# Kernel optimization log

Hardware: AMD Instinct MI355X
Metric: run time of the kernel (lower is better)

Reference implementation:

```python
import jax, jax.numpy as jnp
import numpy as np

HEADS = 4
RATES = (1, 2, 3, 4)
BN_EPS = 1e-5


def setup_inputs() -> dict:
    key = jax.random.key(0)
    k1, k2, k3 = jax.random.split(key, 3)
    b, c, h, w = 4, 256, 128, 128
    x = jax.random.normal(k1, (b, c, h, w), dtype=jnp.float32)
    w_qkv = jax.random.normal(k2, (3 * c, c), dtype=jnp.float32) * 0.02
    w_proj = jax.random.normal(k3, (c, c), dtype=jnp.float32) * 0.02
    gamma = jnp.ones((c,), dtype=jnp.float32)
    beta = jnp.zeros((c,), dtype=jnp.float32)
    return {"x": x, "w_qkv": w_qkv, "w_proj": w_proj, "gamma": gamma, "beta": beta}


def _neighbors(t, r, h, w):
    # t: [b, d, h, w] -> [b, d, 9, h, w], 3x3 dilated window with zero padding
    # (row-major kernel-position order matches F.unfold's C x kh x kw layout).
    tp = jnp.pad(t, ((0, 0), (0, 0), (r, r), (r, r)))
    return jnp.stack(
        [tp[:, :, i * r:i * r + h, j * r:j * r + w] for i in range(3) for j in range(3)],
        axis=2,
    )


def reference(x, w_qkv, w_proj, gamma, beta):
    b, c, h, w = x.shape
    d = c // HEADS
    # 1x1 conv == channel matmul
    qkv = jnp.einsum('oc,bchw->bohw', w_qkv, x)
    q, k, v = jnp.split(qkv, 3, axis=1)
    q = q.reshape(b, HEADS, d, h, w)
    k = k.reshape(b, HEADS, d, h, w)
    v = v.reshape(b, HEADS, d, h, w)
    outs = []
    for hi, r in enumerate(RATES):
        qh = q[:, hi]                      # [b, d, h, w]
        k_n = _neighbors(k[:, hi], r, h, w)  # [b, d, 9, h, w]
        v_n = _neighbors(v[:, hi], r, h, w)  # [b, d, 9, h, w]
        scores = jnp.einsum('bdhw,bdnhw->bnhw', qh, k_n)  # [b, 9, h, w]
        attn = jax.nn.softmax(scores, axis=1)
        outs.append(jnp.einsum('bdnhw,bnhw->bdhw', v_n, attn))
    y = jnp.concatenate(outs, axis=1)      # [b, c, h, w]
    y = jnp.einsum('oc,bchw->bohw', w_proj, y)
    # BatchNorm2d (training-mode batch statistics, biased variance)
    mean = y.mean(axis=(0, 2, 3), keepdims=True)
    var = ((y - mean) ** 2).mean(axis=(0, 2, 3), keepdims=True)
    yn = (y - mean) * jax.lax.rsqrt(var + BN_EPS)
    yn = yn * gamma[None, :, None, None] + beta[None, :, None, None]
    return x + jax.nn.silu(yn)
```

## Files before the change

### kernel.cpp

```cpp
#include <hip/hip_runtime.h>
#include <hip/hip_bf16.h>

#define BATCH 4
#define CCH   256
#define HH    128
#define WW    128
#define HWSZ  (HH * WW)
#define NHEADS 4
#define DHEAD 64
#define KDIM  256
#define PDIM  16384

typedef unsigned short u16;
typedef short bf16x8 __attribute__((ext_vector_type(8)));
typedef float f32x4  __attribute__((ext_vector_type(4)));

__device__ __forceinline__ float bf2f(u16 u) {
    return __uint_as_float(((unsigned)u) << 16);
}
__device__ __forceinline__ u16 f2bf(float f) {
    unsigned u = __float_as_uint(f);
    unsigned r = (u + 0x7fffu + ((u >> 16) & 1u)) >> 16;
    return (u16)r;
}
__device__ __forceinline__ unsigned pack2(float a, float b) {
    return (unsigned)f2bf(a) | ((unsigned)f2bf(b) << 16);
}
__device__ __forceinline__ void gl_lds16(const u16* g, u16* l) {
    __builtin_amdgcn_global_load_lds(
        (const __attribute__((address_space(1))) void*)g,
        (__attribute__((address_space(3))) void*)l, 16, 0, 0);
}

__global__ __launch_bounds__(256) void wconv(
    const float* __restrict__ wq, const float* __restrict__ wp,
    u16* __restrict__ wqb, u16* __restrict__ wpb)
{
    const int i = (blockIdx.x * 256 + threadIdx.x) * 4;
    const float4 v = (i < 196608)
        ? *reinterpret_cast<const float4*>(&wq[i])
        : *reinterpret_cast<const float4*>(&wp[i - 196608]);
    ushort4 o;
    o.x = f2bf(v.x); o.y = f2bf(v.y); o.z = f2bf(v.z); o.w = f2bf(v.w);
    if (i < 196608) *reinterpret_cast<ushort4*>(&wqb[i]) = o;
    else            *reinterpret_cast<ushort4*>(&wpb[i - 196608]) = o;
}

__global__ __launch_bounds__(256) void transpose_x(
    const float* __restrict__ x, u16* __restrict__ XT)
{
    __shared__ float t[32][33];
    const int b  = blockIdx.z;
    const int c0 = blockIdx.y * 32;
    const int p0 = blockIdx.x * 32;
    const int tid = threadIdx.x;

    #pragma unroll
    for (int it = 0; it < 4; ++it) {
        const int r = it * 8 + (tid >> 5);
        const int col = tid & 31;
        t[r][col] = x[((size_t)b * CCH + c0 + r) * HWSZ + p0 + col];
    }
    __syncthreads();
    #pragma unroll
    for (int it = 0; it < 2; ++it) {
        const int prow = it * 16 + (tid >> 4);
        const int cpair = (tid & 15) * 2;
        const float v0 = t[cpair][prow];
        const float v1 = t[cpair + 1][prow];
        ushort2 o; o.x = f2bf(v0); o.y = f2bf(v1);
        *reinterpret_cast<ushort2*>(
            &XT[((size_t)b * HWSZ + p0 + prow) * CCH + c0 + cpair]) = o;
    }
}

__global__ __launch_bounds__(256) void gemm_qkv(
    const u16* __restrict__ A, const u16* __restrict__ B,
    u16* __restrict__ QKVH, long long b_zs)
{
    constexpr int BK = 64;
    constexpr int CTP = 72;
    __shared__ __align__(16) u16 lds[18432];
    u16* As = lds;
    u16* Bs = lds + 8192;

    const int tid  = threadIdx.x;
    const int lane = tid & 63;
    const int w    = tid >> 6;
    const int wm   = w >> 1, wn = w & 1;
    const int o0   = blockIdx.y * 128;
    const int pt   = ((blockIdx.x & 7) << 4) | (blockIdx.x >> 3);
    const int p0   = pt * 128;
    const int z    = blockIdx.z;
    const u16* Bz  = B + (size_t)z * b_zs;

    const int srow  = lane >> 3;
    const int sslot = (lane & 7) ^ srow;

    auto stage = [&](int c0) {
        #pragma unroll
        for (int j = 0; j < 4; ++j) {
            const int q = w * 4 + j;
            const int r = q * 8 + srow;
            gl_lds16(A  + (size_t)(o0 + r) * KDIM + c0 + sslot * 8, As + q * 512);
            gl_lds16(Bz + (size_t)(p0 + r) * KDIM + c0 + sslot * 8, Bs + q * 512);
        }
    };

    f32x4 acc[4][4];
    #pragma unroll
    for (int m = 0; m < 4; ++m)
        #pragma unroll
        for (int n = 0; n < 4; ++n)
            acc[m][n] = (f32x4){0.f, 0.f, 0.f, 0.f};

    stage(0);
    #pragma unroll
    for (int kt = 0; kt < KDIM / BK; ++kt) {
        __syncthreads();
        #pragma unroll
        for (int h = 0; h < 2; ++h) {
            bf16x8 af[4], bfr[4];
            #pragma unroll
            for (int m = 0; m < 4; ++m) {
                const int r  = wm * 64 + m * 16 + (lane & 15);
                const int sl = ((h << 2) | (lane >> 4)) ^ (r & 7);
                af[m] = *reinterpret_cast<const bf16x8*>(As + r * BK + sl * 8);
            }
            #pragma unroll
            for (int n = 0; n < 4; ++n) {
                const int r  = wn * 64 + n * 16 + (lane & 15);
                const int sl = ((h << 2) | (lane >> 4)) ^ (r & 7);
                bfr[n] = *reinterpret_cast<const bf16x8*>(Bs + r * BK + sl * 8);
            }
            #pragma unroll
            for (int m = 0; m < 4; ++m)
                #pragma unroll
                for (int n = 0; n < 4; ++n)
                    acc[m][n] = __builtin_amdgcn_mfma_f32_16x16x32_bf16(
                        af[m], bfr[n], acc[m][n], 0, 0, 0);
        }
        if (kt + 1 < KDIM / BK) {
            __syncthreads();
            stage((kt + 1) * BK);
        }
    }

    __syncthreads();
    u16* Ct = lds;
    const int g = lane >> 4, ln15 = lane & 15;
    #pragma unroll
    for (int m = 0; m < 4; ++m) {
        const int och = m * 16 + g * 4;
        #pragma unroll
        for (int n = 0; n < 4; ++n) {
            const int px = wn * 64 + n * 16 + ln15;
            uint2 w2;
            w2.x = pack2(acc[m][n][0], acc[m][n][1]);
            w2.y = pack2(acc[m][n][2], acc[m][n][3]);
            *reinterpret_cast<uint2*>(&Ct[(wm * 128 + px) * CTP + och]) = w2;
        }
    }
    __syncthreads();

    const int c   = tid & 7;
    const int sl  = (tid >> 3) & 1;
    const int px0 = tid >> 4;
    const int abs_slice = blockIdx.y * 2 + sl;
    const int qkv  = abs_slice >> 2;
    const int head = abs_slice & 3;
    u16* dbase = QKVH + ((size_t)(z * NHEADS + head) * HWSZ) * 192 + qkv * 64 + c * 8;
    #pragma unroll
    for (int pass = 0; pass < 8; ++pass) {
        const int px = px0 + pass * 16;
        const uint4 val = *reinterpret_cast<const uint4*>(
            &Ct[(sl * 128 + px) * CTP + c * 8]);
        *reinterpret_cast<uint4*>(dbase + (size_t)(p0 + px) * 192) = val;
    }
}

__global__ __launch_bounds__(256) void attn4(
    const u16* __restrict__ QKVH, u16* __restrict__ YT)
{
    const int hi  = blockIdx.y;
    const int tid = threadIdx.x;
    const int bxr = blockIdx.x;
    const int bx  = (bxr & 7) * 32 + (bxr >> 3);
    const int p   = bx * 64 + (tid >> 2);
    const int quarter = tid & 3;
    const int yy = p >> 7;
    const int xx = p & 127;
    const int r  = hi + 1;

    const u16* base = QKVH +
        ((size_t)(blockIdx.z * NHEADS + hi) * HWSZ) * 192;

    const uint4* qp = reinterpret_cast<const uint4*>(
        base + (size_t)p * 192 + quarter * 16);
    float qf[16];
    #pragma unroll
    for (int c4 = 0; c4 < 2; ++c4) {
        const uint4 t = qp[c4];
        const unsigned wv[4] = {t.x, t.y, t.z, t.w};
        #pragma unroll
        for (int d = 0; d < 4; ++d) {
            qf[c4 * 8 + d * 2 + 0] = __uint_as_float(wv[d] << 16);
            qf[c4 * 8 + d * 2 + 1] = __uint_as_float(wv[d] & 0xffff0000u);
        }
    }

    int   offs[9];
    float valid[9];
    #pragma unroll
    for (int n = 0; n < 9; ++n) {
        const int dy = (n / 3 - 1) * r;
        const int dx = (n % 3 - 1) * r;
        const int y2 = yy + dy, x2 = xx + dx;
        const bool ok = (y2 >= 0) && (y2 < HH) && (x2 >= 0) && (x2 < WW);
        valid[n] = ok ? 1.f : 0.f;
        const int y2c = min(max(y2, 0), HH - 1);
        const int x2c = min(max(x2, 0), WW - 1);
        offs[n] = y2c * WW + x2c;
    }

    float sc[9];
    #pragma unroll
    for (int n = 0; n < 9; ++n) {
        const uint4* kp = reinterpret_cast<const uint4*>(
            base + (size_t)offs[n] * 192 + 64 + quarter * 16);
        float s = 0.f;
        #pragma unroll
        for (int c4 = 0; c4 < 2; ++c4) {
            const uint4 t = kp[c4];
            const unsigned wv[4] = {t.x, t.y, t.z, t.w};
            #pragma unroll
            for (int d = 0; d < 4; ++d) {
                s += qf[c4 * 8 + d * 2 + 0] * __uint_as_float(wv[d] << 16);
                s += qf[c4 * 8 + d * 2 + 1] * __uint_as_float(wv[d] & 0xffff0000u);
            }
        }
        sc[n] = s;
    }
    #pragma unroll
    for (int n = 0; n < 9; ++n) {
        sc[n] += __shfl_xor(sc[n], 1);
        sc[n] += __shfl_xor(sc[n], 2);
        sc[n] *= valid[n];
    }

    float m = sc[0];
    #pragma unroll
    for (int n = 1; n < 9; ++n) m = fmaxf(m, sc[n]);
    float wgt[9], den = 0.f;
    #pragma unroll
    for (int n = 0; n < 9; ++n) { wgt[n] = __expf(sc[n] - m); den += wgt[n]; }
    const float inv = 1.f / den;
    #pragma unroll
    for (int n = 0; n < 9; ++n) wgt[n] *= inv * valid[n];

    float a[16];
    #pragma unroll
    for (int d = 0; d < 16; ++d) a[d] = 0.f;
    #pragma unroll
    for (int n = 0; n < 9; ++n) {
        const uint4* vp = reinterpret_cast<const uint4*>(
            base + (size_t)offs[n] * 192 + 128 + quarter * 16);
        const float wn_ = wgt[n];
        #pragma unroll
        for (int c4 = 0; c4 < 2; ++c4) {
            const uint4 t = vp[c4];
            const unsigned wv[4] = {t.x, t.y, t.z, t.w};
            #pragma unroll
            for (int d = 0; d < 4; ++d) {
                a[c4 * 8 + d * 2 + 0] += wn_ * __uint_as_float(wv[d] << 16);
                a[c4 * 8 + d * 2 + 1] += wn_ * __uint_as_float(wv[d] & 0xffff0000u);
            }
        }
    }

    u16* outp = YT + ((size_t)blockIdx.z * HWSZ + p) * CCH
                   + hi * DHEAD + quarter * 16;
    #pragma unroll
    for (int c4 = 0; c4 < 2; ++c4) {
        uint4 st;
        st.x = pack2(a[c4 * 8 + 0], a[c4 * 8 + 1]);
        st.y = pack2(a[c4 * 8 + 2], a[c4 * 8 + 3]);
        st.z = pack2(a[c4 * 8 + 4], a[c4 * 8 + 5]);
        st.w = pack2(a[c4 * 8 + 6], a[c4 * 8 + 7]);
        *reinterpret_cast<uint4*>(outp + c4 * 8) = st;
    }
}

__global__ __launch_bounds__(256) void gemm_proj(
    const u16* __restrict__ A, const u16* __restrict__ B,
    u16* __restrict__ YP, long long b_zs,
    float* __restrict__ part, int batch0)
{
    constexpr int BK = 64;
    __shared__ u16 As[128 * BK];
    __shared__ u16 Bs[128 * BK];

    const int tid  = threadIdx.x;
    const int lane = tid & 63;
    const int w    = tid >> 6;
    const int wm   = w >> 1, wn = w & 1;
    const int o0   = blockIdx.y * 128;
    const int pt   = ((blockIdx.x & 7) << 4) | (blockIdx.x >> 3);
    const int p0   = pt * 128;
    const u16* Bz  = B + (size_t)blockIdx.z * b_zs;

    const int srow  = lane >> 3;
    const int sslot = (lane & 7) ^ srow;

    auto stage = [&](int c0) {
        #pragma unroll
        for (int j = 0; j < 4; ++j) {
            const int q = w * 4 + j;
            const int r = q * 8 + srow;
            gl_lds16(A  + (size_t)(o0 + r) * KDIM + c0 + sslot * 8, As + q * 512);
            gl_lds16(Bz + (size_t)(p0 + r) * KDIM + c0 + sslot * 8, Bs + q * 512);
        }
    };

    f32x4 acc[4][4];
    #pragma unroll
    for (int m = 0; m < 4; ++m)
        #pragma unroll
        for (int n = 0; n < 4; ++n)
            acc[m][n] = (f32x4){0.f, 0.f, 0.f, 0.f};

    stage(0);
    #pragma unroll
    for (int kt = 0; kt < KDIM / BK; ++kt) {
        __syncthreads();
        #pragma unroll
        for (int h = 0; h < 2; ++h) {
            bf16x8 af[4], bfr[4];
            #pragma unroll
            for (int m = 0; m < 4; ++m) {
                const int r  = wm * 64 + m * 16 + (lane & 15);
                const int sl = ((h << 2) | (lane >> 4)) ^ (r & 7);
                af[m] = *reinterpret_cast<const bf16x8*>(As + r * BK + sl * 8);
            }
            #pragma unroll
            for (int n = 0; n < 4; ++n) {
                const int r  = wn * 64 + n * 16 + (lane & 15);
                const int sl = ((h << 2) | (lane >> 4)) ^ (r & 7);
                bfr[n] = *reinterpret_cast<const bf16x8*>(Bs + r * BK + sl * 8);
            }
            #pragma unroll
            for (int m = 0; m < 4; ++m)
                #pragma unroll
                for (int n = 0; n < 4; ++n)
                    acc[m][n] = __builtin_amdgcn_mfma_f32_16x16x32_bf16(
                        af[m], bfr[n], acc[m][n], 0, 0, 0);
        }
        if (kt + 1 < KDIM / BK) {
            __syncthreads();
            stage((kt + 1) * BK);
        }
    }

    const int g = lane >> 4, ln15 = lane & 15;
    const int batch = batch0 + blockIdx.z;
    u16* Yz = YP + (size_t)batch * CCH * HWSZ;
    float s[4][4], q2[4][4];
    #pragma unroll
    for (int m = 0; m < 4; ++m) {
        const int ow = o0 + wm * 64 + m * 16 + g * 4;
        #pragma unroll
        for (int j = 0; j < 4; ++j) { s[m][j] = 0.f; q2[m][j] = 0.f; }
        #pragma unroll
        for (int n = 0; n < 4; ++n) {
            const int pc = p0 + wn * 64 + n * 16 + ln15;
            #pragma unroll
            for (int j = 0; j < 4; ++j) {
                const float v = acc[m][n][j];
                Yz[(size_t)(ow + j) * PDIM + pc] = f2bf(v);
                s[m][j]  += v;
                q2[m][j] += v * v;
            }
        }
    }
    #pragma unroll
    for (int mask = 1; mask <= 8; mask <<= 1) {
        #pragma unroll
        for (int m = 0; m < 4; ++m)
            #pragma unroll
            for (int j = 0; j < 4; ++j) {
                s[m][j]  += __shfl_xor(s[m][j],  mask);
                q2[m][j] += __shfl_xor(q2[m][j], mask);
            }
    }
    if (ln15 == 0) {
        const int pxblk = batch * 256 + pt * 2 + wn;
        #pragma unroll
        for (int m = 0; m < 4; ++m) {
            const int ow = o0 + wm * 64 + m * 16 + g * 4;
            #pragma unroll
            for (int j = 0; j < 4; ++j) {
                const size_t idx = ((size_t)(ow + j) * 1024 + pxblk) * 2;
                part[idx]     = s[m][j];
                part[idx + 1] = q2[m][j];
            }
        }
    }
}

__global__ __launch_bounds__(256) void bn_final(
    const float* __restrict__ part, float* __restrict__ stats)
{
    const int c = blockIdx.x;
    const int tid = threadIdx.x;
    float s = 0.f, q = 0.f;
    #pragma unroll
    for (int it = 0; it < 4; ++it) {
        const int i = tid + it * 256;
        s += part[((size_t)c * 1024 + i) * 2 + 0];
        q += part[((size_t)c * 1024 + i) * 2 + 1];
    }
    __shared__ float sh0[256], sh1[256];
    sh0[tid] = s; sh1[tid] = q;
    __syncthreads();
    for (int st = 128; st > 0; st >>= 1) {
        if (tid < st) { sh0[tid] += sh0[tid + st]; sh1[tid] += sh1[tid + st]; }
        __syncthreads();
    }
    if (tid == 0) {
        const float N = (float)(BATCH * HWSZ);
        const float mean = sh0[0] / N;
        const float var  = sh1[0] / N - mean * mean;
        stats[c]       = mean;
        stats[CCH + c] = rsqrtf(var + 1e-5f);
    }
}

__global__ __launch_bounds__(256) void bn_silu_res(
    const u16* __restrict__ yp, const float* __restrict__ x,
    const float* __restrict__ stats, const float* __restrict__ gamma,
    const float* __restrict__ beta, float* __restrict__ out)
{
    const size_t i = ((size_t)blockIdx.x * 256 + threadIdx.x) * 8;
    const int c = (int)((i >> 14) & 255);
    const float mean = stats[c];
    const float inv  = stats[CCH + c];
    const float g = gamma[c], bt = beta[c];

    const uint4 yv = *reinterpret_cast<const uint4*>(&yp[i]);
    const unsigned wv[4] = {yv.x, yv.y, yv.z, yv.w};
    float vo[8];
    #pragma unroll
    for (int d = 0; d < 4; ++d) {
        const float y0 = __uint_as_float(wv[d] << 16);
        const float y1 = __uint_as_float(wv[d] & 0xffff0000u);
        const float yn0 = (y0 - mean) * inv * g + bt;
        const float yn1 = (y1 - mean) * inv * g + bt;
        vo[d * 2 + 0] = yn0 / (1.f + __expf(-yn0));
        vo[d * 2 + 1] = yn1 / (1.f + __expf(-yn1));
    }
    const float4 x0 = *reinterpret_cast<const float4*>(&x[i]);
    const float4 x1 = *reinterpret_cast<const float4*>(&x[i + 4]);
    float4 o0, o1;
    o0.x = x0.x + vo[0]; o0.y = x0.y + vo[1];
    o0.z = x0.z + vo[2]; o0.w = x0.w + vo[3];
    o1.x = x1.x + vo[4]; o1.y = x1.y + vo[5];
    o1.z = x1.z + vo[6]; o1.w = x1.w + vo[7];
    *reinterpret_cast<float4*>(&out[i])     = o0;
    *reinterpret_cast<float4*>(&out[i + 4]) = o1;
}

extern "C" void kernel_launch(void* const* d_in, const int* in_sizes, int n_in,
                              void* d_out, int out_size, void* d_ws, size_t ws_size,
                              hipStream_t stream)
{
    const float* x      = (const float*)d_in[0];
    const float* w_qkv  = (const float*)d_in[1];
    const float* w_proj = (const float*)d_in[2];
    const float* gamma  = (const float*)d_in[3];
    const float* beta   = (const float*)d_in[4];
    float* out = (float*)d_out;

    u16*   XT    = (u16*)d_ws;
    u16*   YP    = XT;
    u16*   WQb   = XT + (size_t)BATCH * HWSZ * CCH;
    u16*   WPb   = WQb + 768 * CCH;
    float* part  = (float*)(WPb + CCH * CCH);
    float* stats = part + (size_t)CCH * 1024 * 2;
    u16*   QKVH  = (u16*)(stats + 512);

    const size_t qkvh_full = (size_t)BATCH * NHEADS * HWSZ * 192;
    const size_t yt_full   = (size_t)BATCH * HWSZ * CCH;
    u16* YT_full = QKVH + qkvh_full;
    u16* YT_pair = QKVH + qkvh_full / 2;

    const size_t need_full =
        (size_t)((char*)(YT_full + yt_full) - (char*)d_ws);

    wconv<<<256, 256, 0, stream>>>(w_qkv, w_proj, WQb, WPb);

    transpose_x<<<dim3(HWSZ / 32, CCH / 32, BATCH), 256, 0, stream>>>(x, XT);

    if (ws_size >= need_full) {
        gemm_qkv<<<dim3(PDIM / 128, 768 / 128, BATCH), 256, 0, stream>>>(
            WQb, XT, QKVH, (long long)HWSZ * CCH);

        attn4<<<dim3(HWSZ / 64, NHEADS, BATCH), 256, 0, stream>>>(QKVH, YT_full);

        gemm_proj<<<dim3(PDIM / 128, CCH / 128, BATCH), 256, 0, stream>>>(
            WPb, YT_full, YP, (long long)HWSZ * CCH, part, 0);
    } else {
        for (int pair = 0; pair < 2; ++pair) {
            const u16* Bx = XT + (size_t)pair * 2 * HWSZ * CCH;
            gemm_qkv<<<dim3(PDIM / 128, 768 / 128, 2), 256, 0, stream>>>(
                WQb, Bx, QKVH, (long long)HWSZ * CCH);

            attn4<<<dim3(HWSZ / 64, NHEADS, 2), 256, 0, stream>>>(QKVH, YT_pair);

            gemm_proj<<<dim3(PDIM / 128, CCH / 128, 2), 256, 0, stream>>>(
                WPb, YT_pair, YP, (long long)HWSZ * CCH, part, pair * 2);
        }
    }

    bn_final<<<CCH, 256, 0, stream>>>(part, stats);

    bn_silu_res<<<(unsigned)((size_t)BATCH * CCH * HWSZ / 8 / 256), 256, 0, stream>>>(
        YP, x, stats, gamma, beta, out);
}
```

Measured before the change: 144.1 us.

## Fuse x transpose and bf16 conversion into QKV GEMM tile loading

Removes the separate transpose_x kernel and makes gemm_qkv read fp32 x in its native channel-major layout, converting to bf16 and writing swizzled B tiles into LDS through registers. This eliminates the intermediate bf16 transposed buffer's write and read and one launch. In exchange each of the six output-channel tiles re-reads fp32 x (twice the bytes of bf16), and staging switches from async global-to-LDS loads to register-prefetched loads that raise register pressure.

```diff
diff --git a/kernel.cpp b/kernel.cpp
--- a/kernel.cpp
+++ b/kernel.cpp
@@ -46,37 +46,9 @@
     else            *reinterpret_cast<ushort4*>(&wpb[i - 196608]) = o;
 }
 
-__global__ __launch_bounds__(256) void transpose_x(
-    const float* __restrict__ x, u16* __restrict__ XT)
-{
-    __shared__ float t[32][33];
-    const int b  = blockIdx.z;
-    const int c0 = blockIdx.y * 32;
-    const int p0 = blockIdx.x * 32;
-    const int tid = threadIdx.x;
-
-    #pragma unroll
-    for (int it = 0; it < 4; ++it) {
-        const int r = it * 8 + (tid >> 5);
-        const int col = tid & 31;
-        t[r][col] = x[((size_t)b * CCH + c0 + r) * HWSZ + p0 + col];
-    }
-    __syncthreads();
-    #pragma unroll
-    for (int it = 0; it < 2; ++it) {
-        const int prow = it * 16 + (tid >> 4);
-        const int cpair = (tid & 15) * 2;
-        const float v0 = t[cpair][prow];
-        const float v1 = t[cpair + 1][prow];
-        ushort2 o; o.x = f2bf(v0); o.y = f2bf(v1);
-        *reinterpret_cast<ushort2*>(
-            &XT[((size_t)b * HWSZ + p0 + prow) * CCH + c0 + cpair]) = o;
-    }
-}
-
 __global__ __launch_bounds__(256) void gemm_qkv(
-    const u16* __restrict__ A, const u16* __restrict__ B,
-    u16* __restrict__ QKVH, long long b_zs)
+    const u16* __restrict__ A, const float* __restrict__ X,
+    u16* __restrict__ QKVH, long long x_zs)
 {
     constexpr int BK = 64;
     constexpr int CTP = 72;
@@ -92,18 +64,52 @@
     const int pt   = ((blockIdx.x & 7) << 4) | (blockIdx.x >> 3);
     const int p0   = pt * 128;
     const int z    = blockIdx.z;
-    const u16* Bz  = B + (size_t)z * b_zs;
+    const float* Xz = X + (size_t)z * x_zs;
 
     const int srow  = lane >> 3;
     const int sslot = (lane & 7) ^ srow;
-
-    auto stage = [&](int c0) {
+    const int px    = tid & 127;
+    const int ob    = (tid >> 7) * 4;
+
+    bf16x8 aReg[4];
+    float  bReg[4][8];
+
+    auto loadA = [&](int c0) {
+        #pragma unroll
+        for (int j = 0; j < 4; ++j) {
+            const int q  = w * 4 + j;
+            const int rr = q * 8 + srow;
+            aReg[j] = *reinterpret_cast<const bf16x8*>(
+                A + (size_t)(o0 + rr) * KDIM + c0 + sslot * 8);
+        }
+    };
+    auto writeA = [&]() {
         #pragma unroll
         for (int j = 0; j < 4; ++j) {
             const int q = w * 4 + j;
-            const int r = q * 8 + srow;
-            gl_lds16(A  + (size_t)(o0 + r) * KDIM + c0 + sslot * 8, As + q * 512);
-            gl_lds16(Bz + (size_t)(p0 + r) * KDIM + c0 + sslot * 8, Bs + q * 512);
+            *reinterpret_cast<bf16x8*>(As + q * 512 + lane * 8) = aReg[j];
+        }
+    };
+    auto loadB = [&](int c0) {
+        #pragma unroll
+        for (int j = 0; j < 4; ++j) {
+            const int o = ob + j;
+            #pragma unroll
+            for (int i = 0; i < 8; ++i)
+                bReg[j][i] = Xz[(size_t)(c0 + o * 8 + i) * HWSZ + p0 + px];
+        }
+    };
+    auto writeB = [&]() {
+        #pragma unroll
+        for (int j = 0; j < 4; ++j) {
+            const int o    = ob + j;
+            const int slot = o ^ (px & 7);
+            uint4 st;
+            st.x = pack2(bReg[j][0], bReg[j][1]);
+            st.y = pack2(bReg[j][2], bReg[j][3]);
+            st.z = pack2(bReg[j][4], bReg[j][5]);
+            st.w = pack2(bReg[j][6], bReg[j][7]);
+            *reinterpret_cast<uint4*>(Bs + px * 64 + slot * 8) = st;
         }
     };
 
@@ -114,9 +120,15 @@
         for (int n = 0; n < 4; ++n)
             acc[m][n] = (f32x4){0.f, 0.f, 0.f, 0.f};
 
-    stage(0);
+    loadA(0); loadB(0);
     #pragma unroll
     for (int kt = 0; kt < KDIM / BK; ++kt) {
+        __syncthreads();
+        writeA(); writeB();
+        if (kt + 1 < KDIM / BK) {
+            loadA((kt + 1) * BK);
+            loadB((kt + 1) * BK);
+        }
         __syncthreads();
         #pragma unroll
         for (int h = 0; h < 2; ++h) {
@@ -140,10 +152,6 @@
                     acc[m][n] = __builtin_amdgcn_mfma_f32_16x16x32_bf16(
                         af[m], bfr[n], acc[m][n], 0, 0, 0);
         }
-        if (kt + 1 < KDIM / BK) {
-            __syncthreads();
-            stage((kt + 1) * BK);
-        }
     }
 
     __syncthreads();
@@ -154,11 +162,11 @@
         const int och = m * 16 + g * 4;
         #pragma unroll
         for (int n = 0; n < 4; ++n) {
-            const int px = wn * 64 + n * 16 + ln15;
+            const int ppx = wn * 64 + n * 16 + ln15;
             uint2 w2;
             w2.x = pack2(acc[m][n][0], acc[m][n][1]);
             w2.y = pack2(acc[m][n][2], acc[m][n][3]);
-            *reinterpret_cast<uint2*>(&Ct[(wm * 128 + px) * CTP + och]) = w2;
+            *reinterpret_cast<uint2*>(&Ct[(wm * 128 + ppx) * CTP + och]) = w2;
         }
     }
     __syncthreads();
@@ -172,10 +180,10 @@
     u16* dbase = QKVH + ((size_t)(z * NHEADS + head) * HWSZ) * 192 + qkv * 64 + c * 8;
     #pragma unroll
     for (int pass = 0; pass < 8; ++pass) {
-        const int px = px0 + pass * 16;
+        const int ppx = px0 + pass * 16;
         const uint4 val = *reinterpret_cast<const uint4*>(
-            &Ct[(sl * 128 + px) * CTP + c * 8]);
-        *reinterpret_cast<uint4*>(dbase + (size_t)(p0 + px) * 192) = val;
+            &Ct[(sl * 128 + ppx) * CTP + c * 8]);
+        *reinterpret_cast<uint4*>(dbase + (size_t)(p0 + ppx) * 192) = val;
     }
 }
 
@@ -480,9 +488,8 @@
     const float* beta   = (const float*)d_in[4];
     float* out = (float*)d_out;
 
-    u16*   XT    = (u16*)d_ws;
-    u16*   YP    = XT;
-    u16*   WQb   = XT + (size_t)BATCH * HWSZ * CCH;
+    u16*   YP    = (u16*)d_ws;
+    u16*   WQb   = YP + (size_t)BATCH * HWSZ * CCH;
     u16*   WPb   = WQb + 768 * CCH;
     float* part  = (float*)(WPb + CCH * CCH);
     float* stats = part + (size_t)CCH * 1024 * 2;
@@ -498,11 +505,9 @@
 
     wconv<<<256, 256, 0, stream>>>(w_qkv, w_proj, WQb, WPb);
 
-    transpose_x<<<dim3(HWSZ / 32, CCH / 32, BATCH), 256, 0, stream>>>(x, XT);
-
     if (ws_size >= need_full) {
         gemm_qkv<<<dim3(PDIM / 128, 768 / 128, BATCH), 256, 0, stream>>>(
-            WQb, XT, QKVH, (long long)HWSZ * CCH);
+            WQb, x, QKVH, (long long)CCH * HWSZ);
 
         attn4<<<dim3(HWSZ / 64, NHEADS, BATCH), 256, 0, stream>>>(QKVH, YT_full);
 
@@ -510,9 +515,9 @@
             WPb, YT_full, YP, (long long)HWSZ * CCH, part, 0);
     } else {
         for (int pair = 0; pair < 2; ++pair) {
-            const u16* Bx = XT + (size_t)pair * 2 * HWSZ * CCH;
+            const float* xb = x + (size_t)pair * 2 * CCH * HWSZ;
             gemm_qkv<<<dim3(PDIM / 128, 768 / 128, 2), 256, 0, stream>>>(
-                WQb, Bx, QKVH, (long long)HWSZ * CCH);
+                WQb, xb, QKVH, (long long)CCH * HWSZ);
 
             attn4<<<dim3(HWSZ / 64, NHEADS, 2), 256, 0, stream>>>(QKVH, YT_pair);
 
```

Result: slower. 150.4 us (+4.4%).
